# Kernel optimization log

Measured on AMD Instinct MI355X. Metric: run time of the kernel, lower is better.

Reference implementation:

```python
import jax, jax.numpy as jnp
import numpy as np

B, S, D, H, G, K = 4, 4096, 1024, 16, 4, 3
DG = D // G   # group channels = 256
DH = D // H   # head channels = 64


def setup_inputs() -> dict:
    key = jax.random.key(0)
    ks = jax.random.split(key, 8)
    def w(k, shape, std=0.02):
        return jax.random.normal(k, shape, jnp.float32) * std
    return {
        "x": jax.random.normal(ks[0], (B, S, D), jnp.float32),
        "Wq": w(ks[1], (D, D)), "bq": jnp.zeros((D,), jnp.float32),
        "Wk": w(ks[2], (D, D)), "bk": jnp.zeros((D,), jnp.float32),
        "Wv": w(ks[3], (D, D)), "bv": jnp.zeros((D,), jnp.float32),
        "Wo": w(ks[4], (D, D)), "bo": jnp.zeros((D,), jnp.float32),
        "Woff1": w(ks[5], (DG, DG, K)), "boff1": jnp.zeros((DG,), jnp.float32),
        "Woff2": w(ks[6], (DG,)),
        "bias_table": w(ks[7], (1, 1, S)),
    }


def reference(x, Wq, bq, Wk, bk, Wv, bv, Wo, bo, Woff1, boff1, Woff2, bias_table):
    bsz, seq, d = x.shape
    scale = d ** (-0.5)
    xc = jnp.transpose(x, (0, 2, 1))  # [B, D, S]

    # 1x1 conv projections == channel GEMMs
    q = jnp.einsum('oc,bcs->bos', Wq, xc) + bq[None, :, None]  # [B, D, S]

    # group: [B*G, DG, S]
    gq = q.reshape(bsz * G, DG, seq)
    # offset head: conv1d(k=3, pad=1) -> conv1d(k=1, no bias) -> [B*G, S]
    h = jax.lax.conv_general_dilated(
        gq, Woff1, window_strides=(1,), padding=((K // 2, K // 2),),
        dimension_numbers=('NCH', 'OIH', 'NCH')) + boff1[None, :, None]
    offset = jnp.einsum('c,bcs->bs', Woff2, h)
    offset = jnp.tanh(offset) * K  # offset_range_factor = kernel

    gx = xc.reshape(bsz * G, DG, seq)  # grouped x

    # faithful replication of _grid_sample_1d: F.grid_sample on feats [N,C,S,1]
    # with grid (x = vgrid_scaled -> width dim of size 1, y = 0 -> height dim of
    # size S), bilinear, zero padding, align_corners=False.
    grid = jnp.arange(seq, dtype=x.dtype)[None, :]
    vgrid_scaled = 2.0 * (grid + offset) / max(seq - 1, 1) - 1.0  # [B*G, S]
    ix = vgrid_scaled / 2.0                 # unnormalized width coord (W=1)
    wx = jnp.clip(1.0 - jnp.abs(ix), 0.0, 1.0)  # bilinear weight on width idx 0
    iy = (seq - 1) / 2.0                    # unnormalized height coord for y=0
    y0 = int(np.floor(iy)); y1 = min(y0 + 1, seq - 1)
    wy1 = float(iy - y0); wy0 = 1.0 - wy1
    feat_c = wy0 * gx[:, :, y0] + wy1 * gx[:, :, y1]  # [B*G, DG]
    x_sampled = feat_c[:, :, None] * wx[:, None, :]   # [B*G, DG, S]
    xs = x_sampled.reshape(bsz, d, seq)               # ungroup -> [B, D, S]

    k = jnp.einsum('oc,bcs->bos', Wk, xs) + bk[None, :, None]
    v = jnp.einsum('oc,bcs->bos', Wv, xs) + bv[None, :, None]

    qh = q.reshape(bsz * H, DH, seq)
    kh = k.reshape(bsz * H, DH, seq)
    vh = v.reshape(bsz * H, DH, seq) + bias_table[:, :, :seq]

    # channel attention: contract over sequence dim (as in the original einsum)
    scores = jnp.einsum('bis,bjs->bij', qh, kh) * scale  # [B*H, DH, DH]
    attn = jax.nn.softmax(scores, axis=-1)
    out = jnp.einsum('bij,bjs->bis', attn, vh)           # [B*H, DH, S]
    out = out.reshape(bsz, d, seq).transpose(0, 2, 1)     # [B, S, D]
    return jnp.einsum('bsd,od->bso', out, Wo) + bo
```

## Files before the change

### kernel.cpp

```cpp
#include <hip/hip_runtime.h>
#include <math.h>

#define BB 4
#define SS 4096
#define DD 1024
#define HH 16
#define GG 4
#define KK 3
#define DG 256
#define DH 64
#define CH 16
#define NCH (SS / CH)

enum : size_t {
  OFF_WEFF  = 0,
  OFF_OFFC  = 1024,
  OFF_WEQ   = 1280,
  OFF_ZT    = 13568,
  OFF_WX    = 210176,
  OFF_XWP   = 275712,
  OFF_XW    = 5518592,
  OFF_XS    = 5534976,
  OFF_SW    = 5539072,
  OFF_FEAT  = 5539328,
  OFF_KF    = 5543424,
  OFF_VF    = 5559808,
  OFF_AV    = 5576192,
  OFF_AB    = 5592576,
  OFF_C2    = 5596672,
  OFF_WAV   = 5600768,
  OFF_WOSUM = 5617152,
  WS_FLOATS = 5618176
};

__device__ __forceinline__ float wred_sum(float v) {
#pragma unroll
  for (int o = 32; o > 0; o >>= 1) v += __shfl_xor(v, o, 64);
  return v;
}
__device__ __forceinline__ float wred_max(float v) {
#pragma unroll
  for (int o = 32; o > 0; o >>= 1) v = fmaxf(v, __shfl_xor(v, o, 64));
  return v;
}

__global__ __launch_bounds__(256) void k_pre(
    const float* __restrict__ x,  const float* __restrict__ Wq, const float* __restrict__ bq,
    const float* __restrict__ Wk, const float* __restrict__ Wv, const float* __restrict__ Wo,
    const float* __restrict__ Woff1, const float* __restrict__ boff1,
    const float* __restrict__ Woff2, float* __restrict__ ws) {
  const int t = threadIdx.x;
  const int lane = t & 63;
  const int wv = t >> 6;
  const int bid = blockIdx.x;
  __shared__ float weff_sh[256];
  __shared__ float red[4][64];

  if (bid < 192) {
    const int j = bid >> 4;
    const int c0 = (bid & 15) * 64;
    const int g = j / 3, kk = j - 3 * g;
    float acc = 0.f;
#pragma unroll 4
    for (int cc = 0; cc < DG; ++cc)
      acc += Woff2[cc] * Woff1[(size_t)(cc * DG + t) * KK + kk];
    weff_sh[t] = acc;
    __syncthreads();
    float a = 0.f;
#pragma unroll 4
    for (int ii = 0; ii < 64; ++ii) {
      const int i = wv * 64 + ii;
      a += weff_sh[i] * Wq[(size_t)(g * DG + i) * DD + c0 + lane];
    }
    red[wv][lane] = a;
    __syncthreads();
    if (wv == 0) {
      const float v = red[0][lane] + red[1][lane] + red[2][lane] + red[3][lane];
      ws[OFF_WEQ + (size_t)j * DD + c0 + lane] = v;
    }
  } else if (bid == 192) {
    if (t < 16) ws[OFF_SW + t] = 0.f;
    float accs = 0.f;
#pragma unroll 4
    for (int cc = 0; cc < DG; ++cc) {
      const float* w1 = Woff1 + (size_t)(cc * DG + t) * KK;
      accs += Woff2[cc] * (w1[0] + w1[1] + w1[2]);
    }
    float be = Woff2[t] * boff1[t];
    be = wred_sum(be);
    if (lane == 0) weff_sh[wv] = be;
    __syncthreads();
    const float beff = weff_sh[0] + weff_sh[1] + weff_sh[2] + weff_sh[3];
#pragma unroll
    for (int g = 0; g < 4; ++g) {
      float a = accs * bq[g * DG + t];
      a = wred_sum(a);
      if (lane == 0) red[g][wv] = a;
    }
    __syncthreads();
    if (t < 4)
      ws[OFF_OFFC + t] = red[t][0] + red[t][1] + red[t][2] + red[t][3] + beff;
  } else if (bid < 1217) {
    const int widx = (bid - 193) * 4 + wv;
    const int g = widx >> 10, o = widx & 1023;
    const float4 ak  = ((const float4*)(Wk + (size_t)o * DD + g * DG))[lane];
    const float4 avv = ((const float4*)(Wv + (size_t)o * DD + g * DG))[lane];
    float kk4[4], vv4[4];
#pragma unroll
    for (int b = 0; b < 4; ++b) {
      const float4 xa = ((const float4*)(x + ((size_t)b * SS + 2047) * DD + g * DG))[lane];
      const float4 xb = ((const float4*)(x + ((size_t)b * SS + 2048) * DD + g * DG))[lane];
      const float fx = 0.5f * (xa.x + xb.x), fy = 0.5f * (xa.y + xb.y);
      const float fz = 0.5f * (xa.z + xb.z), fw = 0.5f * (xa.w + xb.w);
      kk4[b] = ak.x * fx + ak.y * fy + ak.z * fz + ak.w * fw;
      vv4[b] = avv.x * fx + avv.y * fy + avv.z * fz + avv.w * fw;
    }
#pragma unroll
    for (int b = 0; b < 4; ++b) { kk4[b] = wred_sum(kk4[b]); vv4[b] = wred_sum(vv4[b]); }
    if (lane == 0) {
#pragma unroll
      for (int b = 0; b < 4; ++b) {
        ws[OFF_KF + ((size_t)(b * GG + g)) * DD + o] = kk4[b];
        ws[OFF_VF + ((size_t)(b * GG + g)) * DD + o] = vv4[b];
      }
    }
  } else {
    const int o = (bid - 1217) * 4 + wv;
    const float4* wo = (const float4*)(Wo + (size_t)o * DD);
    float v = 0.f;
#pragma unroll
    for (int it = 0; it < 4; ++it) {
      const float4 a = wo[lane + 64 * it];
      v += a.x + a.y + a.z + a.w;
    }
    v = wred_sum(v);
    if (lane == 0) ws[OFF_WOSUM + o] = v;
  }
}

__global__ __launch_bounds__(256, 2) void k_zxw(const float* __restrict__ x,
                                                float* __restrict__ ws) {
  const int t = threadIdx.x;
  const int lane = t & 63;
  const int wv = t >> 6;
  const int b = blockIdx.x >> 8;
  const int chunk = blockIdx.x & 255;
  const int s0 = chunk * CH;
  __shared__ float zl[18][12];
  __shared__ float wxs[64];

  {
    const float* weq = ws + OFF_WEQ;
    float4 w[12][4];
#pragma unroll
    for (int j = 0; j < 12; ++j)
#pragma unroll
      for (int it = 0; it < 4; ++it)
        w[j][it] = *(const float4*)(weq + (size_t)j * DD + 4 * (lane + 64 * it));
    for (int r = wv; r < 18; r += 4) {
      const int s = s0 - 1 + r;
      if (s < 0 || s >= SS) continue;
      const float4* xr = (const float4*)(x + ((size_t)b * SS + s) * DD);
      float4 xv[4];
#pragma unroll
      for (int it = 0; it < 4; ++it) xv[it] = xr[lane + 64 * it];
      float acc[12];
#pragma unroll
      for (int j = 0; j < 12; ++j) {
        float a = 0.f;
#pragma unroll
        for (int it = 0; it < 4; ++it)
          a += xv[it].x * w[j][it].x + xv[it].y * w[j][it].y +
               xv[it].z * w[j][it].z + xv[it].w * w[j][it].w;
        acc[j] = a;
      }
#pragma unroll
      for (int j = 0; j < 12; ++j) acc[j] = wred_sum(acc[j]);
      if (lane == 0) {
#pragma unroll
        for (int j = 0; j < 12; ++j) zl[r][j] = acc[j];
      }
    }
  }
  __syncthreads();

  if (t < 64) {
    const int g = t >> 4, si = t & 15;
    const int s = s0 + si;
    float off = ws[OFF_OFFC + g];
    if (s > 0)      off += zl[si][g * 3 + 0];
    off += zl[si + 1][g * 3 + 1];
    if (s < SS - 1) off += zl[si + 2][g * 3 + 2];
    off = tanhf(off) * (float)KK;
    const float vg = 2.0f * ((float)s + off) / (float)(SS - 1) - 1.0f;
    float wvv = 1.0f - fabsf(0.5f * vg);
    wvv = fminf(fmaxf(wvv, 0.0f), 1.0f);
    wxs[t] = wvv;
    ws[OFF_WX + (size_t)(b * GG + g) * SS + s] = wvv;
  }
  __syncthreads();

  if (t < 4) {
    float sl = 0.f;
#pragma unroll
    for (int si = 0; si < 16; ++si) sl += wxs[t * 16 + si];
    atomicAdd(&ws[OFF_SW + b * GG + t], sl);
  }

  float4 aw[5] = {};
#pragma unroll 4
  for (int si = 0; si < CH; ++si) {
    const int s = s0 + si;
    const float4 f = *(const float4*)(x + (size_t)(b * SS + s) * DD + 4 * t);
    const float w0 = wxs[si], w1 = wxs[16 + si], w2 = wxs[32 + si], w3 = wxs[48 + si];
    aw[0].x += f.x * w0; aw[0].y += f.y * w0; aw[0].z += f.z * w0; aw[0].w += f.w * w0;
    aw[1].x += f.x * w1; aw[1].y += f.y * w1; aw[1].z += f.z * w1; aw[1].w += f.w * w1;
    aw[2].x += f.x * w2; aw[2].y += f.y * w2; aw[2].z += f.z * w2; aw[2].w += f.w * w2;
    aw[3].x += f.x * w3; aw[3].y += f.y * w3; aw[3].z += f.z * w3; aw[3].w += f.w * w3;
    aw[4].x += f.x; aw[4].y += f.y; aw[4].z += f.z; aw[4].w += f.w;
  }
#pragma unroll
  for (int slot = 0; slot < 5; ++slot)
    *(float4*)(ws + OFF_XWP + (((size_t)(b * 5 + slot) * NCH + chunk) * DD) + 4 * t) = aw[slot];
}

__global__ void k_red(float* __restrict__ ws) {
  const int t = threadIdx.x;
  const int lane = t & 63;
  const int wvid = t >> 6;
  __shared__ float red[4][64];
  const int rb = blockIdx.x / 80;
  const int rem = blockIdx.x - rb * 80;
  const int slot = rem >> 4;
  const int c = (rem & 15) * 64 + lane;
  const float* base = ws + OFF_XWP + (size_t)(rb * 5 + slot) * NCH * DD;
  float a = 0.f;
#pragma unroll 8
  for (int ii = 0; ii < 64; ++ii)
    a += base[(size_t)(wvid * 64 + ii) * DD + c];
  red[wvid][lane] = a;
  __syncthreads();
  if (wvid == 0) {
    const float v = red[0][lane] + red[1][lane] + red[2][lane] + red[3][lane];
    if (slot < 4) ws[OFF_XW + ((size_t)(rb * GG + slot)) * DD + c] = v;
    else          ws[OFF_XS + (size_t)rb * DD + c] = v;
  }
}

__global__ void k_mid(const float* __restrict__ Wq, const float* __restrict__ bq,
                      const float* __restrict__ bk, const float* __restrict__ bv,
                      float* __restrict__ ws) {
  const int t = threadIdx.x;
  const int lane = t & 63;
  const int wave = blockIdx.x * 4 + (t >> 6);
  const int ab_ = wave >> 10, I = wave & 1023;
  const float4* wq = (const float4*)(Wq + (size_t)I * DD);
  float4 a[4];
#pragma unroll
  for (int it = 0; it < 4; ++it) a[it] = wq[lane + 64 * it];
  float acc[5] = {0.f, 0.f, 0.f, 0.f, 0.f};
#pragma unroll
  for (int g = 0; g < 4; ++g) {
    const float4* xw = (const float4*)(ws + OFF_XW + (size_t)(ab_ * GG + g) * DD);
#pragma unroll
    for (int it = 0; it < 4; ++it) {
      const float4 c = xw[lane + 64 * it];
      acc[g] += a[it].x * c.x + a[it].y * c.y + a[it].z * c.z + a[it].w * c.w;
    }
  }
  const float4* xs = (const float4*)(ws + OFF_XS + (size_t)ab_ * DD);
#pragma unroll
  for (int it = 0; it < 4; ++it) {
    const float4 c = xs[lane + 64 * it];
    acc[4] += a[it].x * c.x + a[it].y * c.y + a[it].z * c.z + a[it].w * c.w;
  }
#pragma unroll
  for (int u = 0; u < 5; ++u) acc[u] = wred_sum(acc[u]);
  const float bqi = bq[I];
  const float q0 = acc[0] + bqi * ws[OFF_SW + ab_ * GG + 0];
  const float q1 = acc[1] + bqi * ws[OFF_SW + ab_ * GG + 1];
  const float q2 = acc[2] + bqi * ws[OFF_SW + ab_ * GG + 2];
  const float q3 = acc[3] + bqi * ws[OFF_SW + ab_ * GG + 3];
  const float qs = acc[4] + (float)SS * bqi;
  const int J = (I & ~63) | lane;
  const float* Kf = ws + OFF_KF + (size_t)ab_ * GG * DD;
  float sc = q0 * Kf[0 * DD + J] + q1 * Kf[1 * DD + J] +
             q2 * Kf[2 * DD + J] + q3 * Kf[3 * DD + J] + bk[J] * qs;
  sc *= 0.03125f;
  const float m = wred_max(sc);
  const float e = expf(sc - m);
  const float sum = wred_sum(e);
  const float attn = e / sum;
  const float* Vf = ws + OFF_VF + (size_t)ab_ * GG * DD;
#pragma unroll
  for (int g = 0; g < 4; ++g) {
    const float av = wred_sum(attn * Vf[(size_t)g * DD + J]);
    if (lane == 0) ws[OFF_AV + (size_t)wave * 4 + g] = av;
  }
  const float abv = wred_sum(attn * bv[J]);
  if (lane == 0) ws[OFF_AB + wave] = abv;
}

__global__ void k_wav(const float* __restrict__ Wo, const float* __restrict__ bo,
                      float* __restrict__ ws) {
  const int gid = blockIdx.x * blockDim.x + threadIdx.x;
  const int lane = gid & 63;
  const int w = gid >> 6;
  if (w >= BB * DD) return;
  const int b = w >> 10, o = w & 1023;
  float acc0 = 0, acc1 = 0, acc2 = 0, acc3 = 0, acc4 = 0;
  const float4* wo4 = (const float4*)(Wo + (size_t)o * DD);
  const float* AV = ws + OFF_AV + (size_t)b * DD * 4;
  const float* Ab = ws + OFF_AB + (size_t)b * DD;
#pragma unroll
  for (int it = 0; it < 4; ++it) {
    const int d4 = lane + 64 * it;
    const float4 wv4 = wo4[d4];
    const float4 a0 = *(const float4*)(AV + (size_t)(4 * d4 + 0) * 4);
    const float4 a1 = *(const float4*)(AV + (size_t)(4 * d4 + 1) * 4);
    const float4 a2 = *(const float4*)(AV + (size_t)(4 * d4 + 2) * 4);
    const float4 a3 = *(const float4*)(AV + (size_t)(4 * d4 + 3) * 4);
    acc0 += wv4.x * a0.x + wv4.y * a1.x + wv4.z * a2.x + wv4.w * a3.x;
    acc1 += wv4.x * a0.y + wv4.y * a1.y + wv4.z * a2.y + wv4.w * a3.y;
    acc2 += wv4.x * a0.z + wv4.y * a1.z + wv4.z * a2.z + wv4.w * a3.z;
    acc3 += wv4.x * a0.w + wv4.y * a1.w + wv4.z * a2.w + wv4.w * a3.w;
    const float4 abv = *(const float4*)(Ab + 4 * d4);
    acc4 += wv4.x * abv.x + wv4.y * abv.y + wv4.z * abv.z + wv4.w * abv.w;
  }
  acc0 = wred_sum(acc0); acc1 = wred_sum(acc1); acc2 = wred_sum(acc2);
  acc3 = wred_sum(acc3); acc4 = wred_sum(acc4);
  if (lane == 0) {
    float* WAV = ws + OFF_WAV + (size_t)w * 4;
    WAV[0] = acc0; WAV[1] = acc1; WAV[2] = acc2; WAV[3] = acc3;
    ws[OFF_C2 + w] = acc4 + bo[o];
  }
}

__global__ __launch_bounds__(256) void k_out(const float* __restrict__ btab,
                                             const float* __restrict__ ws,
                                             float* __restrict__ out) {
  const int b = blockIdx.x >> 8;
  const int ch = blockIdx.x & 255;
  const int t = threadIdx.x;
  const int o0 = 4 * t;
  float4 wav[4];
#pragma unroll
  for (int io = 0; io < 4; ++io)
    wav[io] = *(const float4*)(ws + OFF_WAV + (size_t)(b * DD + o0 + io) * 4);
  const float4 c24  = *(const float4*)(ws + OFF_C2 + (size_t)b * DD + o0);
  const float4 wos4 = *(const float4*)(ws + OFF_WOSUM + o0);
  const float* wx = ws + OFF_WX;
  const int s0 = ch * CH;
#pragma unroll 2
  for (int si = 0; si < CH; ++si) {
    const int s = s0 + si;
    const float w0 = wx[(size_t)(b * GG + 0) * SS + s];
    const float w1 = wx[(size_t)(b * GG + 1) * SS + s];
    const float w2 = wx[(size_t)(b * GG + 2) * SS + s];
    const float w3 = wx[(size_t)(b * GG + 3) * SS + s];
    const float bt = btab[s];
    float4 val;
    val.x = c24.x + bt * wos4.x + w0 * wav[0].x + w1 * wav[0].y + w2 * wav[0].z + w3 * wav[0].w;
    val.y = c24.y + bt * wos4.y + w0 * wav[1].x + w1 * wav[1].y + w2 * wav[1].z + w3 * wav[1].w;
    val.z = c24.z + bt * wos4.z + w0 * wav[2].x + w1 * wav[2].y + w2 * wav[2].z + w3 * wav[2].w;
    val.w = c24.w + bt * wos4.w + w0 * wav[3].x + w1 * wav[3].y + w2 * wav[3].z + w3 * wav[3].w;
    *(float4*)(out + (size_t)(b * SS + s) * DD + o0) = val;
  }
}

extern "C" void kernel_launch(void* const* d_in, const int* in_sizes, int n_in,
                              void* d_out, int out_size, void* d_ws, size_t ws_size,
                              hipStream_t stream) {
  const float* x     = (const float*)d_in[0];
  const float* Wq    = (const float*)d_in[1];
  const float* bq    = (const float*)d_in[2];
  const float* Wk    = (const float*)d_in[3];
  const float* bk    = (const float*)d_in[4];
  const float* Wv    = (const float*)d_in[5];
  const float* bv    = (const float*)d_in[6];
  const float* Wo    = (const float*)d_in[7];
  const float* bo    = (const float*)d_in[8];
  const float* Woff1 = (const float*)d_in[9];
  const float* boff1 = (const float*)d_in[10];
  const float* Woff2 = (const float*)d_in[11];
  const float* btab  = (const float*)d_in[12];
  float* ws  = (float*)d_ws;
  float* out = (float*)d_out;

  k_pre<<<1473, 256, 0, stream>>>(x, Wq, bq, Wk, Wv, Wo, Woff1, boff1, Woff2, ws);
  k_zxw<<<1024, 256, 0, stream>>>(x, ws);
  k_red<<<320, 256, 0, stream>>>(ws);
  k_mid<<<1024, 256, 0, stream>>>(Wq, bq, bk, bv, ws);
  k_wav<<<1024, 256, 0, stream>>>(Wo, bo, ws);
  k_out<<<1024, 256, 0, stream>>>(btab, ws, out);
}
```

Before: 233.4 us.

## Move independent Wk/Wv/Wo prep blocks into k_zxw, split accumulators, nontemporal output

```diff
diff --git a/kernel.cpp b/kernel.cpp
--- a/kernel.cpp
+++ b/kernel.cpp
@@ -11,6 +11,8 @@
 #define DH 64
 #define CH 16
 #define NCH (SS / CH)
+
+typedef float v4f __attribute__((ext_vector_type(4)));
 
 enum : size_t {
   OFF_WEFF  = 0,
@@ -45,8 +47,7 @@
 }
 
 __global__ __launch_bounds__(256) void k_pre(
-    const float* __restrict__ x,  const float* __restrict__ Wq, const float* __restrict__ bq,
-    const float* __restrict__ Wk, const float* __restrict__ Wv, const float* __restrict__ Wo,
+    const float* __restrict__ Wq, const float* __restrict__ bq,
     const float* __restrict__ Woff1, const float* __restrict__ boff1,
     const float* __restrict__ Woff2, float* __restrict__ ws) {
   const int t = threadIdx.x;
@@ -60,25 +61,30 @@
     const int j = bid >> 4;
     const int c0 = (bid & 15) * 64;
     const int g = j / 3, kk = j - 3 * g;
-    float acc = 0.f;
-#pragma unroll 4
-    for (int cc = 0; cc < DG; ++cc)
-      acc += Woff2[cc] * Woff1[(size_t)(cc * DG + t) * KK + kk];
-    weff_sh[t] = acc;
+    float a0 = 0.f, a1 = 0.f, a2 = 0.f, a3 = 0.f;
+#pragma unroll 8
+    for (int u = 0; u < 64; ++u) {
+      a0 += Woff2[u]       * Woff1[(size_t)((u)       * DG + t) * KK + kk];
+      a1 += Woff2[u + 64]  * Woff1[(size_t)((u + 64)  * DG + t) * KK + kk];
+      a2 += Woff2[u + 128] * Woff1[(size_t)((u + 128) * DG + t) * KK + kk];
+      a3 += Woff2[u + 192] * Woff1[(size_t)((u + 192) * DG + t) * KK + kk];
+    }
+    weff_sh[t] = (a0 + a1) + (a2 + a3);
     __syncthreads();
-    float a = 0.f;
-#pragma unroll 4
-    for (int ii = 0; ii < 64; ++ii) {
+    float b0 = 0.f, b1 = 0.f;
+#pragma unroll 8
+    for (int ii = 0; ii < 32; ++ii) {
       const int i = wv * 64 + ii;
-      a += weff_sh[i] * Wq[(size_t)(g * DG + i) * DD + c0 + lane];
-    }
-    red[wv][lane] = a;
+      b0 += weff_sh[i]      * Wq[(size_t)(g * DG + i)      * DD + c0 + lane];
+      b1 += weff_sh[i + 32] * Wq[(size_t)(g * DG + i + 32) * DD + c0 + lane];
+    }
+    red[wv][lane] = b0 + b1;
     __syncthreads();
     if (wv == 0) {
       const float v = red[0][lane] + red[1][lane] + red[2][lane] + red[3][lane];
       ws[OFF_WEQ + (size_t)j * DD + c0 + lane] = v;
     }
-  } else if (bid == 192) {
+  } else {
     if (t < 16) ws[OFF_SW + t] = 0.f;
     float accs = 0.f;
 #pragma unroll 4
@@ -100,8 +106,23 @@
     __syncthreads();
     if (t < 4)
       ws[OFF_OFFC + t] = red[t][0] + red[t][1] + red[t][2] + red[t][3] + beff;
-  } else if (bid < 1217) {
-    const int widx = (bid - 193) * 4 + wv;
+  }
+}
+
+__global__ __launch_bounds__(256, 2) void k_zxw(const float* __restrict__ x,
+                                                const float* __restrict__ Wk,
+                                                const float* __restrict__ Wv,
+                                                const float* __restrict__ Wo,
+                                                float* __restrict__ ws) {
+  const int t = threadIdx.x;
+  const int lane = t & 63;
+  const int wv = t >> 6;
+  const int bid = blockIdx.x;
+  __shared__ float zl[18][12];
+  __shared__ float wxs[64];
+
+  if (bid < 1024) {
+    const int widx = bid * 4 + wv;
     const int g = widx >> 10, o = widx & 1023;
     const float4 ak  = ((const float4*)(Wk + (size_t)o * DD + g * DG))[lane];
     const float4 avv = ((const float4*)(Wv + (size_t)o * DD + g * DG))[lane];
@@ -124,8 +145,9 @@
         ws[OFF_VF + ((size_t)(b * GG + g)) * DD + o] = vv4[b];
       }
     }
-  } else {
-    const int o = (bid - 1217) * 4 + wv;
+    return;
+  } else if (bid < 1280) {
+    const int o = (bid - 1024) * 4 + wv;
     const float4* wo = (const float4*)(Wo + (size_t)o * DD);
     float v = 0.f;
 #pragma unroll
@@ -135,19 +157,13 @@
     }
     v = wred_sum(v);
     if (lane == 0) ws[OFF_WOSUM + o] = v;
-  }
-}
-
-__global__ __launch_bounds__(256, 2) void k_zxw(const float* __restrict__ x,
-                                                float* __restrict__ ws) {
-  const int t = threadIdx.x;
-  const int lane = t & 63;
-  const int wv = t >> 6;
-  const int b = blockIdx.x >> 8;
-  const int chunk = blockIdx.x & 255;
+    return;
+  }
+
+  const int zbid = bid - 1280;
+  const int b = zbid >> 8;
+  const int chunk = zbid & 255;
   const int s0 = chunk * CH;
-  __shared__ float zl[18][12];
-  __shared__ float wxs[64];
 
   {
     const float* weq = ws + OFF_WEQ;
@@ -359,12 +375,12 @@
     const float w2 = wx[(size_t)(b * GG + 2) * SS + s];
     const float w3 = wx[(size_t)(b * GG + 3) * SS + s];
     const float bt = btab[s];
-    float4 val;
+    v4f val;
     val.x = c24.x + bt * wos4.x + w0 * wav[0].x + w1 * wav[0].y + w2 * wav[0].z + w3 * wav[0].w;
     val.y = c24.y + bt * wos4.y + w0 * wav[1].x + w1 * wav[1].y + w2 * wav[1].z + w3 * wav[1].w;
     val.z = c24.z + bt * wos4.z + w0 * wav[2].x + w1 * wav[2].y + w2 * wav[2].z + w3 * wav[2].w;
     val.w = c24.w + bt * wos4.w + w0 * wav[3].x + w1 * wav[3].y + w2 * wav[3].z + w3 * wav[3].w;
-    *(float4*)(out + (size_t)(b * SS + s) * DD + o0) = val;
+    __builtin_nontemporal_store(val, (v4f*)(out + (size_t)(b * SS + s) * DD + o0));
   }
 }
 
@@ -387,8 +403,8 @@
   float* ws  = (float*)d_ws;
   float* out = (float*)d_out;
 
-  k_pre<<<1473, 256, 0, stream>>>(x, Wq, bq, Wk, Wv, Wo, Woff1, boff1, Woff2, ws);
-  k_zxw<<<1024, 256, 0, stream>>>(x, ws);
+  k_pre<<<193, 256, 0, stream>>>(Wq, bq, Woff1, boff1, Woff2, ws);
+  k_zxw<<<2304, 256, 0, stream>>>(x, Wk, Wv, Wo, ws);
   k_red<<<320, 256, 0, stream>>>(ws);
   k_mid<<<1024, 256, 0, stream>>>(Wq, bq, bk, bv, ws);
   k_wav<<<1024, 256, 0, stream>>>(Wo, bo, ws);
```

New measurement: 213.5 us. 8.5% less time.
